# Kernel tuning notes

Hardware: AMD Instinct MI355X
Metric: run time of the kernel (lower is better)

Reference implementation:

```python
import jax, jax.numpy as jnp
import numpy as np

B, L, D, H = 4, 2048, 512, 8
DK = D // H


def setup_inputs() -> dict:
    key = jax.random.key(0)
    ks = jax.random.split(key, 12)
    s = 1.0 / np.sqrt(D)
    return {
        "q": jax.random.normal(ks[0], (B, L, D), jnp.float32),
        "k": jax.random.normal(ks[1], (B, L, D), jnp.float32),
        "v": jax.random.normal(ks[2], (B, L, D), jnp.float32),
        "masks": jax.random.randint(ks[3], (B, L), 0, 2, jnp.int32),
        "wq_w": jax.random.normal(ks[4], (D, D), jnp.float32) * s,
        "wq_b": jnp.zeros((D,), jnp.float32),
        "wk_w": jax.random.normal(ks[5], (D, D), jnp.float32) * s,
        "wk_b": jnp.zeros((D,), jnp.float32),
        "wv_w": jax.random.normal(ks[6], (D, D), jnp.float32) * s,
        "wv_b": jnp.zeros((D,), jnp.float32),
        "wo_w": jax.random.normal(ks[7], (D, D), jnp.float32) * s,
        "wo_b": jnp.zeros((D,), jnp.float32),
    }


def reference(q, k, v, masks, wq_w, wq_b, wk_w, wk_b, wv_w, wv_b, wo_w, wo_b):
    b, l1, d = q.shape
    l2 = k.shape[1]
    # torch Linear: y = x @ W.T + b; weight shape (out, in)
    qh = (q @ wq_w.T + wq_b).reshape(b, l1, H, DK).transpose(0, 2, 1, 3)  # (B,H,L1,DK)
    kh = (k @ wk_w.T + wk_b).reshape(b, l2, H, DK).transpose(0, 2, 1, 3)  # (B,H,L2,DK)
    vh = (v @ wv_w.T + wv_b).reshape(b, l2, H, DK).transpose(0, 2, 1, 3)  # (B,H,L2,DK)
    scores = jnp.einsum("bhqd,bhkd->bhqk", qh, kh) / np.sqrt(DK).astype(np.float32)
    # 2D encoder mask (B, L2) broadcast over heads and query positions
    neg = jnp.float32(np.finfo(np.float32).min)
    scores = jnp.where(masks[:, None, None, :] == 0, neg, scores)
    weights = jax.nn.softmax(scores, axis=-1)  # dropout_rate=0.0 -> identity
    ctx = jnp.einsum("bhqk,bhkd->bhqd", weights, vh)
    concat = ctx.transpose(0, 2, 1, 3).reshape(b, l1, d)
    return concat @ wo_w.T + wo_b
```

## Files before the change

### kernel.cpp

```cpp
#include <hip/hip_runtime.h>
#include <hip/hip_bf16.h>
#include <cstddef>

typedef __attribute__((ext_vector_type(8)))  short bf16x8;
typedef __attribute__((ext_vector_type(4)))  float f32x4;

constexpr int Bn = 4, Ln = 2048, Dn = 512, Hn = 8, DKn = 64, Mtot = 8192;
constexpr float QSCALE = 0.125f * 1.44269504088896341f;
constexpr size_t HE = (size_t)Bn * Hn * Ln * DKn;
constexpr size_t WN = (size_t)Dn * Dn;

__device__ inline unsigned cvt_pk_bf16(float lo, float hi) {
    unsigned r;
    asm("v_cvt_pk_bf16_f32 %0, %1, %2" : "=v"(r) : "v"(lo), "v"(hi));
    return r;
}
__device__ inline short f2bf(float x) {
    union { float f; unsigned u; } v; v.f = x;
    unsigned r = v.u + 0x7fffu + ((v.u >> 16) & 1u);
    return (short)(r >> 16);
}
__device__ inline void gl_lds16(const short* g, short* l) {
    __builtin_amdgcn_global_load_lds(
        (const __attribute__((address_space(1))) void*)g,
        (__attribute__((address_space(3))) void*)l, 16, 0, 0);
}

__global__ __launch_bounds__(256) void prep_all(
    const float* __restrict__ q, const float* __restrict__ k, const float* __restrict__ v,
    const float* __restrict__ wq, const float* __restrict__ wk,
    const float* __restrict__ wv, const float* __restrict__ wo,
    const int* __restrict__ masks,
    short* __restrict__ Xb, short* __restrict__ Wb, float* __restrict__ maskF)
{
    const size_t NX4 = 3 * HE / 4;
    const size_t NW4 = WN;
    size_t gid = (size_t)blockIdx.x * 256 + threadIdx.x;
    if (gid < NX4) {
        const size_t per = HE / 4;
        int which = (int)(gid >> 20);
        const float* src = (which == 0) ? q : (which == 1) ? k : v;
        size_t i4 = gid & (per - 1);
        float4 xv = *(const float4*)&src[i4 * 4];
        uint2 p = {cvt_pk_bf16(xv.x, xv.y), cvt_pk_bf16(xv.z, xv.w)};
        *(uint2*)&Xb[(size_t)which * HE + i4 * 4] = p;
    } else if (gid < NX4 + NW4) {
        size_t wi4 = gid - NX4;
        const size_t per = WN / 4;
        int which = (int)(wi4 >> 16);
        const float* src = (which == 0) ? wq : (which == 1) ? wk : (which == 2) ? wv : wo;
        size_t i4 = wi4 & (per - 1);
        float4 xv = *(const float4*)&src[i4 * 4];
        uint2 p = {cvt_pk_bf16(xv.x, xv.y), cvt_pk_bf16(xv.z, xv.w)};
        *(uint2*)&Wb[(size_t)which * WN + i4 * 4] = p;
    } else {
        size_t mi = gid - NX4 - NW4;
        if (mi < (size_t)Bn * Ln) maskF[mi] = (masks[mi] == 0) ? -1e30f : 0.f;
    }
}

__global__ __launch_bounds__(256) void mask_prep(
    const int* __restrict__ masks, float* __restrict__ maskF)
{
    int i = blockIdx.x * 256 + threadIdx.x;
    if (i < Bn * Ln) maskF[i] = (masks[i] == 0) ? -1e30f : 0.f;
}

__global__ __launch_bounds__(256) void qkv_proj_bf16(
    const short* __restrict__ Xb, const short* __restrict__ Wb,
    const float* __restrict__ bq, const float* __restrict__ bk, const float* __restrict__ bv,
    short* __restrict__ Qh, short* __restrict__ Kh, short* __restrict__ Vt)
{
    const int p = blockIdx.z;
    const short* X    = Xb + (size_t)p * Mtot * Dn;
    const short* W    = Wb + (size_t)p * Dn * Dn;
    const float* bias = (p == 0) ? bq : (p == 1) ? bk : bv;
    short*       O    = (p == 0) ? Qh : (p == 1) ? Kh : Vt;
    const float scl   = (p == 0) ? QSCALE : 1.0f;

    __shared__ short As[128 * 64];
    __shared__ short Bs[128 * 64];

    const int tid  = threadIdx.x;
    const int lane = tid & 63, w = tid >> 6;
    const int wr = w >> 1, wc = w & 1;
    const int l16 = lane & 15, g = lane >> 4;
    const int m0 = blockIdx.x * 128, n0 = blockIdx.y * 128;

    const short* Ag[4]; const short* Bg[4]; int ldsOff[4];
    #pragma unroll
    for (int f = 0; f < 4; ++f) {
        int c = tid + 256 * f;
        int row = c >> 3, col8 = c & 7;
        int scolw = ((col8 ^ (row & 7)) << 3);
        Ag[f] = X + (size_t)(m0 + row) * Dn + scolw;
        Bg[f] = W + (size_t)(n0 + row) * Dn + scolw;
        ldsOff[f] = (w * 64 + 256 * f) * 8;
    }

    f32x4 acc[4][4];
    #pragma unroll
    for (int i = 0; i < 4; ++i)
        #pragma unroll
        for (int j = 0; j < 4; ++j)
            acc[i][j] = (f32x4){0.f, 0.f, 0.f, 0.f};

    for (int ks = 0; ks < 8; ++ks) {
        #pragma unroll
        for (int f = 0; f < 4; ++f) {
            gl_lds16(Ag[f], &As[ldsOff[f]]);
            gl_lds16(Bg[f], &Bs[ldsOff[f]]);
            Ag[f] += 64; Bg[f] += 64;
        }
        __syncthreads();

        bf16x8 bfv[4][2];
        #pragma unroll
        for (int j = 0; j < 4; ++j) {
            int row = wc * 64 + j * 16 + l16;
            int sw = (row & 7) << 3;
            bfv[j][0] = *(const bf16x8*)&Bs[row * 64 + ((g * 8) ^ sw)];
            bfv[j][1] = *(const bf16x8*)&Bs[row * 64 + ((32 + g * 8) ^ sw)];
        }
        #pragma unroll
        for (int i = 0; i < 4; ++i) {
            int row = wr * 64 + i * 16 + l16;
            int sw = (row & 7) << 3;
            bf16x8 a0 = *(const bf16x8*)&As[row * 64 + ((g * 8) ^ sw)];
            bf16x8 a1 = *(const bf16x8*)&As[row * 64 + ((32 + g * 8) ^ sw)];
            #pragma unroll
            for (int j = 0; j < 4; ++j) {
                acc[i][j] = __builtin_amdgcn_mfma_f32_16x16x32_bf16(a0, bfv[j][0], acc[i][j], 0, 0, 0);
                acc[i][j] = __builtin_amdgcn_mfma_f32_16x16x32_bf16(a1, bfv[j][1], acc[i][j], 0, 0, 0);
            }
        }
        __syncthreads();
    }

    const int bb = m0 >> 11;
    #pragma unroll
    for (int i = 0; i < 4; ++i) {
        #pragma unroll
        for (int j = 0; j < 4; ++j) {
            int n  = n0 + wc * 64 + j * 16 + l16;
            int h  = n >> 6, dk = n & 63;
            float bval = bias[n];
            #pragma unroll
            for (int r = 0; r < 4; ++r) {
                int m  = m0 + wr * 64 + i * 16 + g * 4 + r;
                int lq = m & (Ln - 1);
                short val = f2bf((acc[i][j][r] + bval) * scl);
                if (p < 2)
                    O[(((size_t)bb * Hn + h) * Ln + lq) * DKn + dk] = val;
                else
                    O[(((size_t)bb * Hn + h) * DKn + dk) * Ln + lq] = val;
            }
        }
    }
}

__global__ __launch_bounds__(256) void out_proj_bf16(
    const short* __restrict__ Ctx, const short* __restrict__ Wo,
    const float* __restrict__ bias, float* __restrict__ Out)
{
    __shared__ short As[64 * 64];
    __shared__ short Bs[64 * 64];

    const int tid  = threadIdx.x;
    const int lane = tid & 63, w = tid >> 6;
    const int wr = w >> 1, wc = w & 1;
    const int l16 = lane & 15, g = lane >> 4;
    const int m0 = blockIdx.x * 64, n0 = blockIdx.y * 64;

    const short* Ag[2]; const short* Bg[2]; int ldsOff[2];
    #pragma unroll
    for (int f = 0; f < 2; ++f) {
        int c = tid + 256 * f;
        int row = c >> 3, col8 = c & 7;
        int scolw = ((col8 ^ (row & 7)) << 3);
        Ag[f] = Ctx + (size_t)(m0 + row) * Dn + scolw;
        Bg[f] = Wo  + (size_t)(n0 + row) * Dn + scolw;
        ldsOff[f] = (w * 64 + 256 * f) * 8;
    }

    f32x4 acc[2][2];
    #pragma unroll
    for (int i = 0; i < 2; ++i)
        #pragma unroll
        for (int j = 0; j < 2; ++j)
            acc[i][j] = (f32x4){0.f, 0.f, 0.f, 0.f};

    for (int ks = 0; ks < 8; ++ks) {
        #pragma unroll
        for (int f = 0; f < 2; ++f) {
            gl_lds16(Ag[f], &As[ldsOff[f]]);
            gl_lds16(Bg[f], &Bs[ldsOff[f]]);
            Ag[f] += 64; Bg[f] += 64;
        }
        __syncthreads();

        bf16x8 bfv[2][2];
        #pragma unroll
        for (int j = 0; j < 2; ++j) {
            int row = wc * 32 + j * 16 + l16;
            int sw = (row & 7) << 3;
            bfv[j][0] = *(const bf16x8*)&Bs[row * 64 + ((g * 8) ^ sw)];
            bfv[j][1] = *(const bf16x8*)&Bs[row * 64 + ((32 + g * 8) ^ sw)];
        }
        #pragma unroll
        for (int i = 0; i < 2; ++i) {
            int row = wr * 32 + i * 16 + l16;
            int sw = (row & 7) << 3;
            bf16x8 a0 = *(const bf16x8*)&As[row * 64 + ((g * 8) ^ sw)];
            bf16x8 a1 = *(const bf16x8*)&As[row * 64 + ((32 + g * 8) ^ sw)];
            #pragma unroll
            for (int j = 0; j < 2; ++j) {
                acc[i][j] = __builtin_amdgcn_mfma_f32_16x16x32_bf16(a0, bfv[j][0], acc[i][j], 0, 0, 0);
                acc[i][j] = __builtin_amdgcn_mfma_f32_16x16x32_bf16(a1, bfv[j][1], acc[i][j], 0, 0, 0);
            }
        }
        __syncthreads();
    }

    #pragma unroll
    for (int i = 0; i < 2; ++i) {
        #pragma unroll
        for (int j = 0; j < 2; ++j) {
            int n = n0 + wc * 32 + j * 16 + l16;
            float bval = bias[n];
            #pragma unroll
            for (int r = 0; r < 4; ++r) {
                int m = m0 + wr * 32 + i * 16 + g * 4 + r;
                Out[(size_t)m * Dn + n] = acc[i][j][r] + bval;
            }
        }
    }
}

__global__ __launch_bounds__(256, 3) void attn_mfma(
    const short* __restrict__ Qh, const short* __restrict__ Kh, const short* __restrict__ Vt,
    const float* __restrict__ maskF, short* __restrict__ Ctx)
{
    __shared__ short smem[16384];

    const int tid  = threadIdx.x;
    const int lane = tid & 63, w = tid >> 6;
    const int l16 = lane & 15, g = lane >> 4;
    const int qt = w & 1, hf = w >> 1;

    const int bid = blockIdx.x;
    const int id  = (bid & 7) * 128 + (bid >> 3);
    const int qb  = id & 31;
    const int bh  = id >> 5;
    const int bb  = bh >> 3, hd = bh & 7;
    const int q0  = qb * 64;
    constexpr int NT = 32;

    const short* Qp = Qh + (size_t)bh * Ln * DKn;
    const short* Kp = Kh + (size_t)bh * Ln * DKn;
    const short* Vp = Vt + (size_t)bh * DKn * Ln;
    const float* mp = maskF + bb * Ln + hf * 1024;

    bf16x8 qf[2][2];
    #pragma unroll
    for (int mf = 0; mf < 2; ++mf)
        #pragma unroll
        for (int c = 0; c < 2; ++c)
            qf[mf][c] = *(const bf16x8*)&Qp[(size_t)(q0 + qt * 32 + mf * 16 + l16) * DKn + c * 32 + g * 8];

    constexpr short BF1 = (short)0x3F80;
    const bf16x8 ones = {BF1, BF1, BF1, BF1, BF1, BF1, BF1, BF1};

    const short* kg[2]; const short* vg[2]; int sbk[2];
    #pragma unroll
    for (int j = 0; j < 2; ++j) {
        int sb = qt * 2 + j;
        sbk[j] = sb * 512;
        int p  = sb * 8 + (lane >> 3);
        int kc = ((p & 0x0C) << 1) | ((p & 0x10) >> 2) | (p & 3);
        int scol = ((lane & 7) ^ (p & 7)) << 3;
        kg[j] = Kp + (size_t)(hf * 1024 + kc) * DKn + scol;
        int vrow = sb * 16 + (lane >> 2);
        vg[j] = Vp + (size_t)vrow * Ln + hf * 1024 + (lane & 3) * 8;
    }

    int kofs[2][2];
    #pragma unroll
    for (int kt = 0; kt < 2; ++kt) {
        int row = kt * 16 + l16;
        kofs[kt][0] = row * 64 + ((g * 8) ^ ((row & 7) << 3));
        kofs[kt][1] = row * 64 + ((32 + g * 8) ^ ((row & 7) << 3));
    }
    int vofs[4];
    #pragma unroll
    for (int d = 0; d < 4; ++d)
        vofs[d] = (d * 16 + l16) * 32 + g * 8;

    f32x4 oacc[2][4];
    #pragma unroll
    for (int mf = 0; mf < 2; ++mf)
        #pragma unroll
        for (int d = 0; d < 4; ++d) oacc[mf][d] = (f32x4){0.f, 0.f, 0.f, 0.f};
    f32x4 lsum[2] = {(f32x4){0.f, 0.f, 0.f, 0.f}, (f32x4){0.f, 0.f, 0.f, 0.f}};

    #pragma unroll
    for (int j = 0; j < 2; ++j) {
        gl_lds16(kg[j], smem + hf * 4096 + sbk[j]);
        gl_lds16(vg[j], smem + 8192 + hf * 4096 + sbk[j]);
    }
    __syncthreads();

    int cb = 0;
    for (int t = 0; t < NT; ++t) {
        if (t < NT - 1) {
            const int ko = (t + 1) * 2048;
            const int vo = (t + 1) * 32;
            short* kd = smem + (hf * 2 + (cb ^ 1)) * 2048;
            short* vd = smem + 8192 + (hf * 2 + (cb ^ 1)) * 2048;
            #pragma unroll
            for (int j = 0; j < 2; ++j) {
                gl_lds16(kg[j] + ko, kd + sbk[j]);
                gl_lds16(vg[j] + vo, vd + sbk[j]);
            }
        }
        const short* Kb = smem + (hf * 2 + cb) * 2048;
        const short* Vb = smem + 8192 + (hf * 2 + cb) * 2048;

        f32x4 mk[2];
        mk[0] = *(const f32x4*)&mp[t * 32 + 8 * g];
        mk[1] = *(const f32x4*)&mp[t * 32 + 8 * g + 4];

        bf16x8 kf[2][2];
        #pragma unroll
        for (int kt = 0; kt < 2; ++kt) {
            kf[kt][0] = *(const bf16x8*)&Kb[kofs[kt][0]];
            kf[kt][1] = *(const bf16x8*)&Kb[kofs[kt][1]];
        }

        f32x4 sv[2][2];
        __builtin_amdgcn_s_setprio(1);
        #pragma unroll
        for (int mf = 0; mf < 2; ++mf)
            #pragma unroll
            for (int kt = 0; kt < 2; ++kt) {
                f32x4 z = __builtin_amdgcn_mfma_f32_16x16x32_bf16(kf[kt][0], qf[mf][0], mk[kt], 0, 0, 0);
                z = __builtin_amdgcn_mfma_f32_16x16x32_bf16(kf[kt][1], qf[mf][1], z, 0, 0, 0);
                sv[mf][kt] = z;
            }
        __builtin_amdgcn_s_setprio(0);

        bf16x8 pf[2];
        #pragma unroll
        for (int mf = 0; mf < 2; ++mf) {
            float e0 = exp2f(sv[mf][0][0]), e1 = exp2f(sv[mf][0][1]);
            float e2 = exp2f(sv[mf][0][2]), e3 = exp2f(sv[mf][0][3]);
            float e4 = exp2f(sv[mf][1][0]), e5 = exp2f(sv[mf][1][1]);
            float e6 = exp2f(sv[mf][1][2]), e7 = exp2f(sv[mf][1][3]);
            union { unsigned u[4]; bf16x8 v; } pu;
            pu.u[0] = cvt_pk_bf16(e0, e1);
            pu.u[1] = cvt_pk_bf16(e2, e3);
            pu.u[2] = cvt_pk_bf16(e4, e5);
            pu.u[3] = cvt_pk_bf16(e6, e7);
            pf[mf] = pu.v;
        }

        bf16x8 vf[4];
        #pragma unroll
        for (int d = 0; d < 4; ++d)
            vf[d] = *(const bf16x8*)&Vb[vofs[d]];

        __builtin_amdgcn_s_setprio(1);
        #pragma unroll
        for (int mf = 0; mf < 2; ++mf) {
            lsum[mf] = __builtin_amdgcn_mfma_f32_16x16x32_bf16(ones, pf[mf], lsum[mf], 0, 0, 0);
            #pragma unroll
            for (int d = 0; d < 4; ++d)
                oacc[mf][d] = __builtin_amdgcn_mfma_f32_16x16x32_bf16(vf[d], pf[mf], oacc[mf][d], 0, 0, 0);
        }
        __builtin_amdgcn_s_setprio(0);

        __syncthreads();
        cb ^= 1;
    }

    float* M = (float*)smem;
    if (hf == 1) {
        #pragma unroll
        for (int mf = 0; mf < 2; ++mf) {
            int ql = qt * 32 + mf * 16 + l16;
            #pragma unroll
            for (int d = 0; d < 4; ++d)
                *(f32x4*)&M[ql * 68 + d * 16 + g * 4] = oacc[mf][d];
            if (g == 0) M[ql * 68 + 64] = lsum[mf][0];
        }
    }
    __syncthreads();
    if (hf == 0) {
        #pragma unroll
        for (int mf = 0; mf < 2; ++mf) {
            int ql = qt * 32 + mf * 16 + l16;
            float lt = lsum[mf][0] + M[ql * 68 + 64];
            float inv = 1.0f / lt;
            size_t mrow = (size_t)bb * Ln + q0 + ql;
            #pragma unroll
            for (int d = 0; d < 4; ++d) {
                f32x4 ob = *(const f32x4*)&M[ql * 68 + d * 16 + g * 4];
                float o0 = (oacc[mf][d][0] + ob[0]) * inv;
                float o1 = (oacc[mf][d][1] + ob[1]) * inv;
                float o2 = (oacc[mf][d][2] + ob[2]) * inv;
                float o3 = (oacc[mf][d][3] + ob[3]) * inv;
                uint2 pr = {cvt_pk_bf16(o0, o1), cvt_pk_bf16(o2, o3)};
                *(uint2*)&Ctx[mrow * Dn + hd * 64 + d * 16 + g * 4] = pr;
            }
        }
    }
}

__global__ __launch_bounds__(256) void qkv_proj_mfma(
    const float* __restrict__ q, const float* __restrict__ k, const float* __restrict__ v,
    const float* __restrict__ wq, const float* __restrict__ wk, const float* __restrict__ wv,
    const float* __restrict__ bq, const float* __restrict__ bk, const float* __restrict__ bv,
    short* __restrict__ Qh, short* __restrict__ Kh, short* __restrict__ Vt)
{
    const int p = blockIdx.z;
    const float* X    = (p == 0) ? q  : (p == 1) ? k  : v;
    const float* W    = (p == 0) ? wq : (p == 1) ? wk : wv;
    const float* bias = (p == 0) ? bq : (p == 1) ? bk : bv;
    short*       O    = (p == 0) ? Qh : (p == 1) ? Kh : Vt;
    const float scl   = (p == 0) ? QSCALE : 1.0f;

    __shared__ short As[128 * 72];
    __shared__ short Bs[128 * 72];

    const int tid  = threadIdx.x;
    const int lane = tid & 63, w = tid >> 6;
    const int wr = w >> 1, wc = w & 1;
    const int l16 = lane & 15, g = lane >> 4;
    const int m0 = blockIdx.x * 128, n0 = blockIdx.y * 128;

    f32x4 acc[4][4];
    #pragma unroll
    for (int i = 0; i < 4; ++i)
        #pragma unroll
        for (int j = 0; j < 4; ++j)
            acc[i][j] = (f32x4){0.f, 0.f, 0.f, 0.f};

    for (int k0 = 0; k0 < Dn; k0 += 64) {
        #pragma unroll
        for (int f = 0; f < 8; ++f) {
            int lin = tid + 256 * f;
            int row = lin >> 4, c4 = lin & 15;
            float4 xv = *(const float4*)&X[(size_t)(m0 + row) * Dn + k0 + c4 * 4];
            uint2 xp = {cvt_pk_bf16(xv.x, xv.y), cvt_pk_bf16(xv.z, xv.w)};
            *(uint2*)&As[row * 72 + c4 * 4] = xp;
            float4 wv4 = *(const float4*)&W[(size_t)(n0 + row) * Dn + k0 + c4 * 4];
            uint2 wp = {cvt_pk_bf16(wv4.x, wv4.y), cvt_pk_bf16(wv4.z, wv4.w)};
            *(uint2*)&Bs[row * 72 + c4 * 4] = wp;
        }
        __syncthreads();

        bf16x8 af[4][2], bfv[4][2];
        #pragma unroll
        for (int i = 0; i < 4; ++i)
            #pragma unroll
            for (int c = 0; c < 2; ++c)
                af[i][c] = *(const bf16x8*)&As[(wr * 64 + i * 16 + l16) * 72 + c * 32 + g * 8];
        #pragma unroll
        for (int j = 0; j < 4; ++j)
            #pragma unroll
            for (int c = 0; c < 2; ++c)
                bfv[j][c] = *(const bf16x8*)&Bs[(wc * 64 + j * 16 + l16) * 72 + c * 32 + g * 8];

        #pragma unroll
        for (int i = 0; i < 4; ++i)
            #pragma unroll
            for (int j = 0; j < 4; ++j) {
                acc[i][j] = __builtin_amdgcn_mfma_f32_16x16x32_bf16(af[i][0], bfv[j][0], acc[i][j], 0, 0, 0);
                acc[i][j] = __builtin_amdgcn_mfma_f32_16x16x32_bf16(af[i][1], bfv[j][1], acc[i][j], 0, 0, 0);
            }
        __syncthreads();
    }

    const int bb = m0 >> 11;
    #pragma unroll
    for (int i = 0; i < 4; ++i) {
        #pragma unroll
        for (int j = 0; j < 4; ++j) {
            int n  = n0 + wc * 64 + j * 16 + l16;
            int h  = n >> 6, dk = n & 63;
            float bval = bias[n];
            #pragma unroll
            for (int r = 0; r < 4; ++r) {
                int m  = m0 + wr * 64 + i * 16 + g * 4 + r;
                int lq = m & (Ln - 1);
                short val = f2bf((acc[i][j][r] + bval) * scl);
                if (p < 2)
                    O[(((size_t)bb * Hn + h) * Ln + lq) * DKn + dk] = val;
                else
                    O[(((size_t)bb * Hn + h) * DKn + dk) * Ln + lq] = val;
            }
        }
    }
}

__global__ __launch_bounds__(256) void out_proj_mfma(
    const short* __restrict__ Ctx, const float* __restrict__ W,
    const float* __restrict__ bias, float* __restrict__ Out)
{
    __shared__ short As[128 * 72];
    __shared__ short Bs[128 * 72];

    const int tid  = threadIdx.x;
    const int lane = tid & 63, w = tid >> 6;
    const int wr = w >> 1, wc = w & 1;
    const int l16 = lane & 15, g = lane >> 4;
    const int m0 = blockIdx.x * 128, n0 = blockIdx.y * 128;

    f32x4 acc[4][4];
    #pragma unroll
    for (int i = 0; i < 4; ++i)
        #pragma unroll
        for (int j = 0; j < 4; ++j)
            acc[i][j] = (f32x4){0.f, 0.f, 0.f, 0.f};

    for (int k0 = 0; k0 < Dn; k0 += 64) {
        #pragma unroll
        for (int f = 0; f < 4; ++f) {
            int lin = tid + 256 * f;
            int row = lin >> 3, c8 = lin & 7;
            bf16x8 av = *(const bf16x8*)&Ctx[(size_t)(m0 + row) * Dn + k0 + c8 * 8];
            *(bf16x8*)&As[row * 72 + c8 * 8] = av;
        }
        #pragma unroll
        for (int f = 0; f < 8; ++f) {
            int lin = tid + 256 * f;
            int row = lin >> 4, c4 = lin & 15;
            float4 wv4 = *(const float4*)&W[(size_t)(n0 + row) * Dn + k0 + c4 * 4];
            uint2 wp = {cvt_pk_bf16(wv4.x, wv4.y), cvt_pk_bf16(wv4.z, wv4.w)};
            *(uint2*)&Bs[row * 72 + c4 * 4] = wp;
        }
        __syncthreads();

        bf16x8 af[4][2], bfv[4][2];
        #pragma unroll
        for (int i = 0; i < 4; ++i)
            #pragma unroll
            for (int c = 0; c < 2; ++c)
                af[i][c] = *(const bf16x8*)&As[(wr * 64 + i * 16 + l16) * 72 + c * 32 + g * 8];
        #pragma unroll
        for (int j = 0; j < 4; ++j)
            #pragma unroll
            for (int c = 0; c < 2; ++c)
                bfv[j][c] = *(const bf16x8*)&Bs[(wc * 64 + j * 16 + l16) * 72 + c * 32 + g * 8];

        #pragma unroll
        for (int i = 0; i < 4; ++i)
            #pragma unroll
            for (int j = 0; j < 4; ++j) {
                acc[i][j] = __builtin_amdgcn_mfma_f32_16x16x32_bf16(af[i][0], bfv[j][0], acc[i][j], 0, 0, 0);
                acc[i][j] = __builtin_amdgcn_mfma_f32_16x16x32_bf16(af[i][1], bfv[j][1], acc[i][j], 0, 0, 0);
            }
        __syncthreads();
    }

    #pragma unroll
    for (int i = 0; i < 4; ++i) {
        #pragma unroll
        for (int j = 0; j < 4; ++j) {
            int n = n0 + wc * 64 + j * 16 + l16;
            float bval = bias[n];
            #pragma unroll
            for (int r = 0; r < 4; ++r) {
                int m = m0 + wr * 64 + i * 16 + g * 4 + r;
                Out[(size_t)m * Dn + n] = acc[i][j][r] + bval;
            }
        }
    }
}

extern "C" void kernel_launch(void* const* d_in, const int* in_sizes, int n_in,
                              void* d_out, int out_size, void* d_ws, size_t ws_size,
                              hipStream_t stream)
{
    (void)in_sizes; (void)n_in; (void)out_size;
    const float* q    = (const float*)d_in[0];
    const float* k    = (const float*)d_in[1];
    const float* v    = (const float*)d_in[2];
    const int*   mks  = (const int*)  d_in[3];
    const float* wq_w = (const float*)d_in[4];
    const float* wq_b = (const float*)d_in[5];
    const float* wk_w = (const float*)d_in[6];
    const float* wk_b = (const float*)d_in[7];
    const float* wv_w = (const float*)d_in[8];
    const float* wv_b = (const float*)d_in[9];
    const float* wo_w = (const float*)d_in[10];
    const float* wo_b = (const float*)d_in[11];
    float* out = (float*)d_out;

    short* ws = (short*)d_ws;
    const size_t needed = (6 * HE + 4 * WN + 2 * (size_t)Bn * Ln) * 2;

    if (ws_size >= needed) {
        short* Xb   = ws;
        short* Ctx  = ws;
        short* Qh   = ws + 3 * HE;
        short* Kh   = ws + 4 * HE;
        short* Vt   = ws + 5 * HE;
        short* Wb   = ws + 6 * HE;
        float* maskF = (float*)(ws + 6 * HE + 4 * WN);

        const int prepBlocks = (int)((3 * HE / 4 + WN + (size_t)Bn * Ln + 255) / 256);
        prep_all<<<dim3(prepBlocks), 256, 0, stream>>>(
            q, k, v, wq_w, wk_w, wv_w, wo_w, mks, Xb, Wb, maskF);

        qkv_proj_bf16<<<dim3(64, 4, 3), 256, 0, stream>>>(
            Xb, Wb, wq_b, wk_b, wv_b, Qh, Kh, Vt);

        attn_mfma<<<dim3(1024), 256, 0, stream>>>(Qh, Kh, Vt, maskF, Ctx);

        out_proj_bf16<<<dim3(128, 8), 256, 0, stream>>>(Ctx, Wb + 3 * WN, wo_b, out);
    } else {
        short* Qh  = ws;
        short* Kh  = ws + HE;
        short* Vt  = ws + 2 * HE;
        short* Ctx = ws + 3 * HE;
        float* maskF = (float*)(ws + 4 * HE);

        mask_prep<<<dim3(32), 256, 0, stream>>>(mks, maskF);
        qkv_proj_mfma<<<dim3(Mtot / 128, Dn / 128, 3), 256, 0, stream>>>(
            q, k, v, wq_w, wk_w, wv_w, wq_b, wk_b, wv_b, Qh, Kh, Vt);
        attn_mfma<<<dim3(1024), 256, 0, stream>>>(Qh, Kh, Vt, maskF, Ctx);
        out_proj_mfma<<<dim3(Mtot / 128, Dn / 128), 256, 0, stream>>>(Ctx, wo_w, wo_b, out);
    }
}
```

Baseline: 114.9 us.

## Read V fragments directly from global, double key tile size per iteration

Result: slower. 311.6 us (+171.3%).

```diff
diff --git a/kernel.cpp b/kernel.cpp
--- a/kernel.cpp
+++ b/kernel.cpp
@@ -237,11 +237,11 @@
     }
 }
 
-__global__ __launch_bounds__(256, 3) void attn_mfma(
+__global__ __launch_bounds__(256, 4) void attn_mfma(
     const short* __restrict__ Qh, const short* __restrict__ Kh, const short* __restrict__ Vt,
     const float* __restrict__ maskF, short* __restrict__ Ctx)
 {
-    __shared__ short smem[16384];
+    __shared__ short Ksm[2][2][64 * 64];
 
     const int tid  = threadIdx.x;
     const int lane = tid & 63, w = tid >> 6;
@@ -254,7 +254,7 @@
     const int bh  = id >> 5;
     const int bb  = bh >> 3, hd = bh & 7;
     const int q0  = qb * 64;
-    constexpr int NT = 32;
+    constexpr int NT = 16;
 
     const short* Qp = Qh + (size_t)bh * Ln * DKn;
     const short* Kp = Kh + (size_t)bh * Ln * DKn;
@@ -271,30 +271,29 @@
     constexpr short BF1 = (short)0x3F80;
     const bf16x8 ones = {BF1, BF1, BF1, BF1, BF1, BF1, BF1, BF1};
 
-    const short* kg[2]; const short* vg[2]; int sbk[2];
-    #pragma unroll
-    for (int j = 0; j < 2; ++j) {
-        int sb = qt * 2 + j;
+    const short* kg[4]; int sbk[4];
+    #pragma unroll
+    for (int j = 0; j < 4; ++j) {
+        int sb = qt * 4 + j;
         sbk[j] = sb * 512;
         int p  = sb * 8 + (lane >> 3);
-        int kc = ((p & 0x0C) << 1) | ((p & 0x10) >> 2) | (p & 3);
+        int kc = (p & 0x20) | ((p & 0x0C) << 1) | ((p & 0x10) >> 2) | (p & 3);
         int scol = ((lane & 7) ^ (p & 7)) << 3;
         kg[j] = Kp + (size_t)(hf * 1024 + kc) * DKn + scol;
-        int vrow = sb * 16 + (lane >> 2);
-        vg[j] = Vp + (size_t)vrow * Ln + hf * 1024 + (lane & 3) * 8;
-    }
-
-    int kofs[2][2];
-    #pragma unroll
-    for (int kt = 0; kt < 2; ++kt) {
+    }
+
+    const short* vgp[4];
+    #pragma unroll
+    for (int d = 0; d < 4; ++d)
+        vgp[d] = Vp + (size_t)(d * 16 + l16) * Ln + hf * 1024 + g * 8;
+
+    int kofs[4][2];
+    #pragma unroll
+    for (int kt = 0; kt < 4; ++kt) {
         int row = kt * 16 + l16;
         kofs[kt][0] = row * 64 + ((g * 8) ^ ((row & 7) << 3));
         kofs[kt][1] = row * 64 + ((32 + g * 8) ^ ((row & 7) << 3));
     }
-    int vofs[4];
-    #pragma unroll
-    for (int d = 0; d < 4; ++d)
-        vofs[d] = (d * 16 + l16) * 32 + g * 8;
 
     f32x4 oacc[2][4];
     #pragma unroll
@@ -304,78 +303,79 @@
     f32x4 lsum[2] = {(f32x4){0.f, 0.f, 0.f, 0.f}, (f32x4){0.f, 0.f, 0.f, 0.f}};
 
     #pragma unroll
-    for (int j = 0; j < 2; ++j) {
-        gl_lds16(kg[j], smem + hf * 4096 + sbk[j]);
-        gl_lds16(vg[j], smem + 8192 + hf * 4096 + sbk[j]);
-    }
+    for (int j = 0; j < 4; ++j)
+        gl_lds16(kg[j], &Ksm[hf][0][sbk[j]]);
     __syncthreads();
 
     int cb = 0;
     for (int t = 0; t < NT; ++t) {
+        bf16x8 vf[4][2];
+        #pragma unroll
+        for (int d = 0; d < 4; ++d) {
+            vf[d][0] = *(const bf16x8*)&vgp[d][t * 64];
+            vf[d][1] = *(const bf16x8*)&vgp[d][t * 64 + 32];
+        }
+
         if (t < NT - 1) {
-            const int ko = (t + 1) * 2048;
-            const int vo = (t + 1) * 32;
-            short* kd = smem + (hf * 2 + (cb ^ 1)) * 2048;
-            short* vd = smem + 8192 + (hf * 2 + (cb ^ 1)) * 2048;
-            #pragma unroll
-            for (int j = 0; j < 2; ++j) {
-                gl_lds16(kg[j] + ko, kd + sbk[j]);
-                gl_lds16(vg[j] + vo, vd + sbk[j]);
-            }
-        }
-        const short* Kb = smem + (hf * 2 + cb) * 2048;
-        const short* Vb = smem + 8192 + (hf * 2 + cb) * 2048;
-
-        f32x4 mk[2];
-        mk[0] = *(const f32x4*)&mp[t * 32 + 8 * g];
-        mk[1] = *(const f32x4*)&mp[t * 32 + 8 * g + 4];
-
-        bf16x8 kf[2][2];
-        #pragma unroll
-        for (int kt = 0; kt < 2; ++kt) {
+            const int ko = (t + 1) * (64 * DKn);
+            #pragma unroll
+            for (int j = 0; j < 4; ++j)
+                gl_lds16(kg[j] + ko, &Ksm[hf][cb ^ 1][sbk[j]]);
+        }
+
+        f32x4 mk[4];
+        mk[0] = *(const f32x4*)&mp[t * 64 + 8 * g];
+        mk[1] = *(const f32x4*)&mp[t * 64 + 8 * g + 4];
+        mk[2] = *(const f32x4*)&mp[t * 64 + 32 + 8 * g];
+        mk[3] = *(const f32x4*)&mp[t * 64 + 32 + 8 * g + 4];
+
+        const short* Kb = Ksm[hf][cb];
+        bf16x8 kf[4][2];
+        #pragma unroll
+        for (int kt = 0; kt < 4; ++kt) {
             kf[kt][0] = *(const bf16x8*)&Kb[kofs[kt][0]];
             kf[kt][1] = *(const bf16x8*)&Kb[kofs[kt][1]];
         }
 
-        f32x4 sv[2][2];
+        f32x4 sv[2][4];
         __builtin_amdgcn_s_setprio(1);
         #pragma unroll
         for (int mf = 0; mf < 2; ++mf)
             #pragma unroll
-            for (int kt = 0; kt < 2; ++kt) {
+            for (int kt = 0; kt < 4; ++kt) {
                 f32x4 z = __builtin_amdgcn_mfma_f32_16x16x32_bf16(kf[kt][0], qf[mf][0], mk[kt], 0, 0, 0);
                 z = __builtin_amdgcn_mfma_f32_16x16x32_bf16(kf[kt][1], qf[mf][1], z, 0, 0, 0);
                 sv[mf][kt] = z;
             }
         __builtin_amdgcn_s_setprio(0);
 
-        bf16x8 pf[2];
+        bf16x8 pf[2][2];
+        #pragma unroll
+        for (int mf = 0; mf < 2; ++mf)
+            #pragma unroll
+            for (int cc = 0; cc < 2; ++cc) {
+                float e0 = exp2f(sv[mf][2 * cc][0]), e1 = exp2f(sv[mf][2 * cc][1]);
+                float e2 = exp2f(sv[mf][2 * cc][2]), e3 = exp2f(sv[mf][2 * cc][3]);
+                float e4 = exp2f(sv[mf][2 * cc + 1][0]), e5 = exp2f(sv[mf][2 * cc + 1][1]);
+                float e6 = exp2f(sv[mf][2 * cc + 1][2]), e7 = exp2f(sv[mf][2 * cc + 1][3]);
+                union { unsigned u[4]; bf16x8 v; } pu;
+                pu.u[0] = cvt_pk_bf16(e0, e1);
+                pu.u[1] = cvt_pk_bf16(e2, e3);
+                pu.u[2] = cvt_pk_bf16(e4, e5);
+                pu.u[3] = cvt_pk_bf16(e6, e7);
+                pf[mf][cc] = pu.v;
+            }
+
+        __builtin_amdgcn_s_setprio(1);
         #pragma unroll
         for (int mf = 0; mf < 2; ++mf) {
-            float e0 = exp2f(sv[mf][0][0]), e1 = exp2f(sv[mf][0][1]);
-            float e2 = exp2f(sv[mf][0][2]), e3 = exp2f(sv[mf][0][3]);
-            float e4 = exp2f(sv[mf][1][0]), e5 = exp2f(sv[mf][1][1]);
-            float e6 = exp2f(sv[mf][1][2]), e7 = exp2f(sv[mf][1][3]);
-            union { unsigned u[4]; bf16x8 v; } pu;
-            pu.u[0] = cvt_pk_bf16(e0, e1);
-            pu.u[1] = cvt_pk_bf16(e2, e3);
-            pu.u[2] = cvt_pk_bf16(e4, e5);
-            pu.u[3] = cvt_pk_bf16(e6, e7);
-            pf[mf] = pu.v;
-        }
-
-        bf16x8 vf[4];
-        #pragma unroll
-        for (int d = 0; d < 4; ++d)
-            vf[d] = *(const bf16x8*)&Vb[vofs[d]];
-
-        __builtin_amdgcn_s_setprio(1);
-        #pragma unroll
-        for (int mf = 0; mf < 2; ++mf) {
-            lsum[mf] = __builtin_amdgcn_mfma_f32_16x16x32_bf16(ones, pf[mf], lsum[mf], 0, 0, 0);
-            #pragma unroll
-            for (int d = 0; d < 4; ++d)
-                oacc[mf][d] = __builtin_amdgcn_mfma_f32_16x16x32_bf16(vf[d], pf[mf], oacc[mf][d], 0, 0, 0);
+            #pragma unroll
+            for (int cc = 0; cc < 2; ++cc) {
+                lsum[mf] = __builtin_amdgcn_mfma_f32_16x16x32_bf16(ones, pf[mf][cc], lsum[mf], 0, 0, 0);
+                #pragma unroll
+                for (int d = 0; d < 4; ++d)
+                    oacc[mf][d] = __builtin_amdgcn_mfma_f32_16x16x32_bf16(vf[d][cc], pf[mf][cc], oacc[mf][d], 0, 0, 0);
+            }
         }
         __builtin_amdgcn_s_setprio(0);
 
@@ -383,7 +383,7 @@
         cb ^= 1;
     }
 
-    float* M = (float*)smem;
+    float* M = (float*)Ksm;
     if (hf == 1) {
         #pragma unroll
         for (int mf = 0; mf < 2; ++mf) {
```
